# Optimization experiments

Hardware: AMD Instinct MI355X
Metric: run time of the kernel (lower is better)

Reference implementation:

```python
import jax, jax.numpy as jnp
import numpy as np

IN_DIM = 256
FF = 512
OUT_DIM = 256
BN_EPS = 1e-5


def setup_inputs() -> dict:
    key = jax.random.key(0)
    ks = jax.random.split(key, 9)
    s = lambda k, shape, fan: jax.random.normal(k, shape, dtype=jnp.float32) / np.sqrt(fan)
    return {
        "inputs": jax.random.normal(ks[0], (4, IN_DIM, 16, 16, 16), dtype=jnp.float32),
        "Wk": s(ks[1], (FF, IN_DIM), IN_DIM),
        "bk": jnp.zeros((FF,), jnp.float32),
        "Wq": s(ks[2], (FF, IN_DIM), IN_DIM),
        "bq": jnp.zeros((FF,), jnp.float32),
        "Wv": s(ks[3], (FF, IN_DIM), IN_DIM),
        "bv": jnp.zeros((FF,), jnp.float32),
        "Wo": s(ks[4], (OUT_DIM, FF), FF),
        "bo": jnp.zeros((OUT_DIM,), jnp.float32),
        "gamma": jnp.ones((OUT_DIM,), jnp.float32),
        "beta": jnp.zeros((OUT_DIM,), jnp.float32),
    }


def reference(inputs, Wk, bk, Wq, bq, Wv, bv, Wo, bo, gamma, beta):
    B, Cin, T, H, W = inputs.shape
    # 1x1x1 Conv3d == pointwise channel projection
    proj = lambda Wt, bt: jnp.einsum("oc,bcthw->bothw", Wt, inputs) + bt[None, :, None, None, None]
    K, Q, V = proj(Wk, bk), proj(Wq, bq), proj(Wv, bv)
    C = K.shape[1]
    N = T * H * W
    Kf = K.reshape(B, C, N)
    Qf = Q.reshape(B, C, N)
    Vf = V.reshape(B, C, N)
    # KQ[b,i,j] = sum_c K[b,c,i] Q[b,c,j], scaled by sqrt(in_dim) (per original)
    KQ = jnp.einsum("bci,bcj->bij", Kf, Qf) / jnp.sqrt(jnp.asarray(Cin, jnp.float32))
    attn = jax.nn.softmax(KQ, axis=2)  # (B, N, N)
    # Original: sum_j V[b,c,i] * attn[b,i,j]  ==  V[b,c,i] * rowsum(attn)[b,i]
    # (we avoid materializing the (B,C,N,N) broadcast tensor)
    row = attn.sum(axis=2)  # (B, N), ~1 numerically but kept for faithfulness
    Vagg = (Vf * row[:, None, :]).reshape(B, C, T, H, W)
    V1 = jax.nn.relu(Vagg)
    out = jnp.einsum("oc,bcthw->bothw", Wo, V1) + bo[None, :, None, None, None]
    res = inputs + jax.nn.relu(out)
    # BatchNorm3d in training mode: batch stats over (B, T, H, W) per channel
    mean = res.mean(axis=(0, 2, 3, 4), keepdims=True)
    var = res.var(axis=(0, 2, 3, 4), keepdims=True)
    xhat = (res - mean) * jax.lax.rsqrt(var + BN_EPS)
    return gamma[None, :, None, None, None] * xhat + beta[None, :, None, None, None]
```

## Files before the change

kernel.cpp:

```cpp
#include <hip/hip_runtime.h>

#define NTOT 4096
#define NB   4
#define CIN  256
#define FF   512
#define COUT 256
#define BN_EPS 1e-5f
#define NT_B 32
#define OSP  36

typedef __attribute__((ext_vector_type(8))) short bf16x8;
typedef __attribute__((ext_vector_type(4))) float f32x4;
typedef unsigned short u16;

#define MFMA16(A, B, C) __builtin_amdgcn_mfma_f32_16x16x32_bf16((A), (B), (C), 0, 0, 0)

__device__ __forceinline__ u16 f2bf(float f) {
    unsigned u = __float_as_uint(f);
    u += 0x7fffu + ((u >> 16) & 1u);
    return (u16)(u >> 16);
}
__device__ __forceinline__ float bf2f(u16 h) {
    return __uint_as_float(((unsigned)h) << 16);
}

__global__ __launch_bounds__(256)
void prep_weights(const float* __restrict__ Wv, const float* __restrict__ Wo,
                  u16* __restrict__ Wvh, u16* __restrict__ Wvl,
                  u16* __restrict__ Woh, u16* __restrict__ Wol,
                  float* __restrict__ stats)
{
    const int t = threadIdx.x;
    const int g = blockIdx.x * 256 + t;
    if (blockIdx.x == 0) { stats[t] = 0.f; stats[256 + t] = 0.f; }

    const float* src; u16 *dh, *dl; int m, kg, K;
    if (g < 16384) { m = g >> 5;           kg = g & 31; K = CIN; src = Wv; dh = Wvh; dl = Wvl; }
    else           { int g2 = g - 16384; m = g2 >> 6; kg = g2 & 63; K = FF;  src = Wo; dh = Woh; dl = Wol; }

    const int nkg = K >> 3;
    const size_t gran = ((size_t)(m >> 4) * nkg + kg) * 16 + (m & 15);
    float4 v0 = *(const float4*)&src[(size_t)m * K + kg * 8];
    float4 v1 = *(const float4*)&src[(size_t)m * K + kg * 8 + 4];
    const float f[8] = {v0.x, v0.y, v0.z, v0.w, v1.x, v1.y, v1.z, v1.w};
    u16 h[8], l[8];
    #pragma unroll
    for (int j = 0; j < 8; ++j) { h[j] = f2bf(f[j]); l[j] = f2bf(f[j] - bf2f(h[j])); }
    bf16x8 hv = {(short)h[0],(short)h[1],(short)h[2],(short)h[3],(short)h[4],(short)h[5],(short)h[6],(short)h[7]};
    bf16x8 lv = {(short)l[0],(short)l[1],(short)l[2],(short)l[3],(short)l[4],(short)l[5],(short)l[6],(short)l[7]};
    *(bf16x8*)&dh[gran * 8] = hv;
    *(bf16x8*)&dl[gran * 8] = lv;
}

__global__ __launch_bounds__(256)
void pack_x(const float* __restrict__ x, u16* __restrict__ xh, u16* __restrict__ xl)
{
    __shared__ float xt[CIN][68];
    const int t = threadIdx.x;
    const int b = blockIdx.x >> 6, tb = blockIdx.x & 63;
    const int n0 = tb * 64;
    const int c16 = t >> 4, tok4 = (t & 15) * 4;

    #pragma unroll
    for (int rr = 0; rr < 16; ++rr) {
        const int c = rr * 16 + c16;
        float4 v = *(const float4*)&x[((size_t)b * CIN + c) * NTOT + n0 + tok4];
        *(float4*)&xt[c][tok4] = v;
    }
    __syncthreads();

    const int tok = t & 63, wq = t >> 6;
    const int sb = tok >> 5, tok32 = tok & 31;
    #pragma unroll
    for (int r = 0; r < 8; ++r) {
        const int kg = r * 4 + wq;
        u16 h8[8], l8[8];
        #pragma unroll
        for (int j = 0; j < 8; ++j) {
            float f = xt[kg * 8 + j][tok];
            h8[j] = f2bf(f);
            l8[j] = f2bf(f - bf2f(h8[j]));
        }
        const size_t e = ((((size_t)(b * 128 + tb * 2 + sb)) * 32 + kg) * 32 + tok32) * 8;
        bf16x8 hv = {(short)h8[0],(short)h8[1],(short)h8[2],(short)h8[3],(short)h8[4],(short)h8[5],(short)h8[6],(short)h8[7]};
        bf16x8 lv = {(short)l8[0],(short)l8[1],(short)l8[2],(short)l8[3],(short)l8[4],(short)l8[5],(short)l8[6],(short)l8[7]};
        *(bf16x8*)&xh[e] = hv;
        *(bf16x8*)&xl[e] = lv;
    }
}

__global__ __launch_bounds__(512, 4)
void fused_mlp(const u16* __restrict__ xh, const u16* __restrict__ xl,
               const u16* __restrict__ Wvh, const u16* __restrict__ Wvl,
               const u16* __restrict__ Woh, const u16* __restrict__ Wol,
               const float* __restrict__ bv, const float* __restrict__ bo,
               const float* __restrict__ x, float* __restrict__ out,
               float* __restrict__ stats)
{
    __shared__ __align__(16) unsigned char smem[65536];
    u16*   xsh = (u16*)smem;
    u16*   xsl = (u16*)(smem + 16384);
    u16*   hsh = (u16*)smem;
    u16*   hsl = (u16*)(smem + 32768);
    float* os  = (float*)smem;

    const int t   = threadIdx.x;
    const int b   = blockIdx.x >> 7;
    const int tb2 = blockIdx.x & 127;
    const int n0  = tb2 * NT_B;
    const int ln  = t & 63, w = t >> 6;
    const int l15 = ln & 15, hi = ln >> 4;

    const size_t xbase = ((size_t)(b * 128 + tb2)) * 8192;
    #pragma unroll
    for (int i = 0; i < 2; ++i) {
        const int e = (i * 512 + t) * 8;
        *(bf16x8*)&xsh[e] = *(const bf16x8*)&xh[xbase + e];
        *(bf16x8*)&xsl[e] = *(const bf16x8*)&xl[xbase + e];
    }

    f32x4 acc1[4][2];
    #pragma unroll
    for (int mt = 0; mt < 4; ++mt)
        #pragma unroll
        for (int nt = 0; nt < 2; ++nt)
            acc1[mt][nt] = (f32x4){0.f, 0.f, 0.f, 0.f};

#define LDW1(KS, P, WH, WL) do { _Pragma("unroll")                              \
    for (int i_ = 0; i_ < 2; ++i_) {                                            \
        const int mt_ = (P) * 2 + i_;                                           \
        const size_t g_ = ((size_t)(w * 4 + mt_) * 32 + (KS) * 4 + hi) * 16 + l15; \
        WH[i_] = *(const bf16x8*)&Wvh[g_ * 8];                                  \
        WL[i_] = *(const bf16x8*)&Wvl[g_ * 8];                                  \
    } } while (0)
#define LDB1(KS, BH, BL) do { _Pragma("unroll")                                 \
    for (int nt_ = 0; nt_ < 2; ++nt_) {                                         \
        const int g_ = ((KS) * 4 + hi) * 32 + nt_ * 16 + l15;                   \
        BH[nt_] = *(const bf16x8*)&xsh[g_ * 8];                                 \
        BL[nt_] = *(const bf16x8*)&xsl[g_ * 8];                                 \
    } } while (0)
#define MM1(P, WH, WL, BH, BL) do { _Pragma("unroll")                           \
    for (int i_ = 0; i_ < 2; ++i_) { _Pragma("unroll")                          \
        for (int nt_ = 0; nt_ < 2; ++nt_) {                                     \
            acc1[(P)*2+i_][nt_] = MFMA16(WH[i_], BH[nt_], acc1[(P)*2+i_][nt_]); \
            acc1[(P)*2+i_][nt_] = MFMA16(WH[i_], BL[nt_], acc1[(P)*2+i_][nt_]); \
            acc1[(P)*2+i_][nt_] = MFMA16(WL[i_], BH[nt_], acc1[(P)*2+i_][nt_]); \
    } } } while (0)

    bf16x8 w1hA[2], w1lA[2], w1hB[2], w1lB[2];
    bf16x8 b1hE[2], b1lE[2], b1hO[2], b1lO[2];

    LDW1(0, 0, w1hA, w1lA);
    __syncthreads();
    LDB1(0, b1hE, b1lE);

    #pragma unroll
    for (int s = 0; s < 16; ++s) {
        const int ks = s >> 1, p = s & 1;
        if (p == 0) {
            LDW1(ks, 1, w1hB, w1lB);
        } else if (ks < 7) {
            LDW1(ks + 1, 0, w1hA, w1lA);
            if (ks & 1) { LDB1(ks + 1, b1hE, b1lE); }
            else        { LDB1(ks + 1, b1hO, b1lO); }
        }
        if (p == 0) {
            if (ks & 1) MM1(0, w1hA, w1lA, b1hO, b1lO);
            else        MM1(0, w1hA, w1lA, b1hE, b1lE);
        } else {
            if (ks & 1) MM1(1, w1hB, w1lB, b1hO, b1lO);
            else        MM1(1, w1hB, w1lB, b1hE, b1lE);
        }
    }
#undef LDW1
#undef LDB1
#undef MM1

#define LDW2(KS, WH, WL) do { _Pragma("unroll")                                 \
    for (int mt_ = 0; mt_ < 2; ++mt_) {                                         \
        const size_t g_ = ((size_t)(w * 2 + mt_) * 64 + (KS) * 4 + hi) * 16 + l15; \
        WH[mt_] = *(const bf16x8*)&Woh[g_ * 8];                                 \
        WL[mt_] = *(const bf16x8*)&Wol[g_ * 8];                                 \
    } } while (0)
#define LDB2(KS, BH, BL) do { _Pragma("unroll")                                 \
    for (int nt_ = 0; nt_ < 2; ++nt_) {                                         \
        const int g_ = ((KS) * 4 + hi) * 32 + nt_ * 16 + l15;                   \
        BH[nt_] = *(const bf16x8*)&hsh[g_ * 8];                                 \
        BL[nt_] = *(const bf16x8*)&hsl[g_ * 8];                                 \
    } } while (0)
#define MM2(WH, WL, BH, BL) do { _Pragma("unroll")                              \
    for (int mt_ = 0; mt_ < 2; ++mt_) { _Pragma("unroll")                       \
        for (int nt_ = 0; nt_ < 2; ++nt_) {                                     \
            acc2[mt_][nt_] = MFMA16(WH[mt_], BH[nt_], acc2[mt_][nt_]);          \
            acc2[mt_][nt_] = MFMA16(WH[mt_], BL[nt_], acc2[mt_][nt_]);          \
            acc2[mt_][nt_] = MFMA16(WL[mt_], BH[nt_], acc2[mt_][nt_]);          \
    } } } while (0)

    bf16x8 w2hA[2], w2lA[2], w2hB[2], w2lB[2];
    bf16x8 b2hE[2], b2lE[2], b2hO[2], b2lO[2];
    LDW2(0, w2hA, w2lA);

    __syncthreads();

    #pragma unroll
    for (int mt = 0; mt < 4; ++mt) {
        const int ff0 = w * 64 + mt * 16 + hi * 4;
        float4 bia = *(const float4*)&bv[ff0];
        const float bb[4] = {bia.x, bia.y, bia.z, bia.w};
        const int kg = ff0 >> 3;
        const int jo = (hi & 1) * 4;
        #pragma unroll
        for (int nt = 0; nt < 2; ++nt) {
            const int tok = nt * 16 + l15;
            u16 hh[4], hl[4];
            #pragma unroll
            for (int r = 0; r < 4; ++r) {
                float v = fmaxf(acc1[mt][nt][r] + bb[r], 0.f);
                hh[r] = f2bf(v);
                hl[r] = f2bf(v - bf2f(hh[r]));
            }
            const int e = (kg * 32 + tok) * 8 + jo;
            *(ushort4*)&hsh[e] = (ushort4){hh[0], hh[1], hh[2], hh[3]};
            *(ushort4*)&hsl[e] = (ushort4){hl[0], hl[1], hl[2], hl[3]};
        }
    }
    __syncthreads();

    f32x4 acc2[2][2];
    #pragma unroll
    for (int mt = 0; mt < 2; ++mt)
        #pragma unroll
        for (int nt = 0; nt < 2; ++nt)
            acc2[mt][nt] = (f32x4){0.f, 0.f, 0.f, 0.f};

    LDB2(0, b2hE, b2lE);
    #pragma unroll
    for (int ks = 0; ks < 16; ++ks) {
        if (ks < 15) {
            if (ks & 1) { LDW2(ks + 1, w2hA, w2lA); LDB2(ks + 1, b2hE, b2lE); }
            else        { LDW2(ks + 1, w2hB, w2lB); LDB2(ks + 1, b2hO, b2lO); }
        }
        if (ks & 1) MM2(w2hB, w2lB, b2hO, b2lO);
        else        MM2(w2hA, w2lA, b2hE, b2lE);
    }
#undef LDW2
#undef LDB2
#undef MM2

    __syncthreads();

    #pragma unroll
    for (int mt = 0; mt < 2; ++mt) {
        const int ch0 = w * 32 + mt * 16 + hi * 4;
        float4 bia = *(const float4*)&bo[ch0];
        const float bb[4] = {bia.x, bia.y, bia.z, bia.w};
        #pragma unroll
        for (int nt = 0; nt < 2; ++nt) {
            const int tok = nt * 16 + l15;
            #pragma unroll
            for (int r = 0; r < 4; ++r)
                os[(ch0 + r) * OSP + tok] = fmaxf(acc2[mt][nt][r] + bb[r], 0.f);
        }
    }
    __syncthreads();

    const int tok4 = (t & 7) * 4;
    const int chb  = t >> 3;
    #pragma unroll
    for (int ii = 0; ii < 4; ++ii) {
        const int ch = chb + ii * 64;
        float4 o = *(float4*)&os[ch * OSP + tok4];
        const size_t goff = ((size_t)b * COUT + ch) * NTOT + n0 + tok4;
        float4 rx = *(const float4*)&x[goff];
        float4 v = {o.x + rx.x, o.y + rx.y, o.z + rx.z, o.w + rx.w};
        *(float4*)&out[goff] = v;
        float s  = v.x + v.y + v.z + v.w;
        float s2 = v.x * v.x + v.y * v.y + v.z * v.z + v.w * v.w;
        #pragma unroll
        for (int off = 1; off < 8; off <<= 1) {
            s  += __shfl_xor(s, off);
            s2 += __shfl_xor(s2, off);
        }
        if ((t & 7) == 0) {
            atomicAdd(&stats[ch], s);
            atomicAdd(&stats[COUT + ch], s2);
        }
    }
}

__global__ __launch_bounds__(256)
void bn_norm(float* __restrict__ out, const float* __restrict__ stats,
             const float* __restrict__ gamma, const float* __restrict__ beta)
{
    const int i4 = blockIdx.x * 256 + threadIdx.x;
    const int c = (i4 >> 10) & (COUT - 1);
    const float inv = 1.0f / (NB * NTOT);
    const float mean = stats[c] * inv;
    const float var  = stats[COUT + c] * inv - mean * mean;
    const float sc = gamma[c] * rsqrtf(var + BN_EPS);
    const float sh = beta[c] - mean * sc;
    float4 v = reinterpret_cast<float4*>(out)[i4];
    v.x = v.x * sc + sh;
    v.y = v.y * sc + sh;
    v.z = v.z * sc + sh;
    v.w = v.w * sc + sh;
    reinterpret_cast<float4*>(out)[i4] = v;
}

extern "C" void kernel_launch(void* const* d_in, const int* in_sizes, int n_in,
                              void* d_out, int out_size, void* d_ws, size_t ws_size,
                              hipStream_t stream)
{
    const float* x     = (const float*)d_in[0];
    const float* Wv    = (const float*)d_in[5];
    const float* bv    = (const float*)d_in[6];
    const float* Wo    = (const float*)d_in[7];
    const float* bo    = (const float*)d_in[8];
    const float* gamma = (const float*)d_in[9];
    const float* beta  = (const float*)d_in[10];
    float* out = (float*)d_out;

    u16* xh   = (u16*)d_ws;
    u16* xl   = xh  + (size_t)NB * NTOT * CIN;
    u16* Wvh  = xl  + (size_t)NB * NTOT * CIN;
    u16* Wvl  = Wvh + (size_t)FF * CIN;
    u16* Woh  = Wvl + (size_t)FF * CIN;
    u16* Wol  = Woh + (size_t)COUT * FF;
    float* stats = (float*)(Wol + (size_t)COUT * FF);

    prep_weights<<<128, 256, 0, stream>>>(Wv, Wo, Wvh, Wvl, Woh, Wol, stats);
    pack_x<<<NB * 64, 256, 0, stream>>>(x, xh, xl);
    fused_mlp<<<NB * 128, 512, 0, stream>>>(xh, xl, Wvh, Wvl, Woh, Wol,
                                            bv, bo, x, out, stats);
    bn_norm<<<(NB * COUT * NTOT / 4) / 256, 256, 0, stream>>>(out, stats, gamma, beta);
}
```

Before: 159.0 us.

## Fuse x bf16 hi/lo packing into fused_mlp and drop pack_x kernel

Removes the separate pack_x kernel and instead has each fused_mlp block load its fp32 input tile straight from global memory into shared memory, then split it into bf16 hi/lo parts in LDS before the MFMA loop. This cuts one kernel launch and the global write and re-read of the packed hi/lo buffers. In exchange it adds an extra __syncthreads and conversion work inside the main kernel, and puts the raw tile and the packed tiles in LDS at the same time.

```diff
diff --git a/kernel.cpp b/kernel.cpp
--- a/kernel.cpp
+++ b/kernel.cpp
@@ -52,54 +52,17 @@
     *(bf16x8*)&dl[gran * 8] = lv;
 }
 
-__global__ __launch_bounds__(256)
-void pack_x(const float* __restrict__ x, u16* __restrict__ xh, u16* __restrict__ xl)
-{
-    __shared__ float xt[CIN][68];
-    const int t = threadIdx.x;
-    const int b = blockIdx.x >> 6, tb = blockIdx.x & 63;
-    const int n0 = tb * 64;
-    const int c16 = t >> 4, tok4 = (t & 15) * 4;
-
-    #pragma unroll
-    for (int rr = 0; rr < 16; ++rr) {
-        const int c = rr * 16 + c16;
-        float4 v = *(const float4*)&x[((size_t)b * CIN + c) * NTOT + n0 + tok4];
-        *(float4*)&xt[c][tok4] = v;
-    }
-    __syncthreads();
-
-    const int tok = t & 63, wq = t >> 6;
-    const int sb = tok >> 5, tok32 = tok & 31;
-    #pragma unroll
-    for (int r = 0; r < 8; ++r) {
-        const int kg = r * 4 + wq;
-        u16 h8[8], l8[8];
-        #pragma unroll
-        for (int j = 0; j < 8; ++j) {
-            float f = xt[kg * 8 + j][tok];
-            h8[j] = f2bf(f);
-            l8[j] = f2bf(f - bf2f(h8[j]));
-        }
-        const size_t e = ((((size_t)(b * 128 + tb * 2 + sb)) * 32 + kg) * 32 + tok32) * 8;
-        bf16x8 hv = {(short)h8[0],(short)h8[1],(short)h8[2],(short)h8[3],(short)h8[4],(short)h8[5],(short)h8[6],(short)h8[7]};
-        bf16x8 lv = {(short)l8[0],(short)l8[1],(short)l8[2],(short)l8[3],(short)l8[4],(short)l8[5],(short)l8[6],(short)l8[7]};
-        *(bf16x8*)&xh[e] = hv;
-        *(bf16x8*)&xl[e] = lv;
-    }
-}
-
 __global__ __launch_bounds__(512, 4)
-void fused_mlp(const u16* __restrict__ xh, const u16* __restrict__ xl,
+void fused_mlp(const float* __restrict__ x,
                const u16* __restrict__ Wvh, const u16* __restrict__ Wvl,
                const u16* __restrict__ Woh, const u16* __restrict__ Wol,
                const float* __restrict__ bv, const float* __restrict__ bo,
-               const float* __restrict__ x, float* __restrict__ out,
-               float* __restrict__ stats)
+               float* __restrict__ out, float* __restrict__ stats)
 {
     __shared__ __align__(16) unsigned char smem[65536];
-    u16*   xsh = (u16*)smem;
-    u16*   xsl = (u16*)(smem + 16384);
+    float* xt  = (float*)smem;
+    u16*   xsh = (u16*)(smem + 32768);
+    u16*   xsl = (u16*)(smem + 49152);
     u16*   hsh = (u16*)smem;
     u16*   hsl = (u16*)(smem + 32768);
     float* os  = (float*)smem;
@@ -111,20 +74,13 @@
     const int ln  = t & 63, w = t >> 6;
     const int l15 = ln & 15, hi = ln >> 4;
 
-    const size_t xbase = ((size_t)(b * 128 + tb2)) * 8192;
-    #pragma unroll
-    for (int i = 0; i < 2; ++i) {
-        const int e = (i * 512 + t) * 8;
-        *(bf16x8*)&xsh[e] = *(const bf16x8*)&xh[xbase + e];
-        *(bf16x8*)&xsl[e] = *(const bf16x8*)&xl[xbase + e];
-    }
-
-    f32x4 acc1[4][2];
-    #pragma unroll
-    for (int mt = 0; mt < 4; ++mt)
-        #pragma unroll
-        for (int nt = 0; nt < 2; ++nt)
-            acc1[mt][nt] = (f32x4){0.f, 0.f, 0.f, 0.f};
+    #pragma unroll
+    for (int i = 0; i < 4; ++i) {
+        const int f4 = t + i * 512;
+        const int c = f4 >> 3, col4 = (f4 & 7) * 4;
+        float4 v = *(const float4*)&x[((size_t)b * CIN + c) * NTOT + n0 + col4];
+        *(float4*)&xt[c * NT_B + col4] = v;
+    }
 
 #define LDW1(KS, P, WH, WL) do { _Pragma("unroll")                              \
     for (int i_ = 0; i_ < 2; ++i_) {                                            \
@@ -133,6 +89,39 @@
         WH[i_] = *(const bf16x8*)&Wvh[g_ * 8];                                  \
         WL[i_] = *(const bf16x8*)&Wvl[g_ * 8];                                  \
     } } while (0)
+
+    bf16x8 w1hA[2], w1lA[2], w1hB[2], w1lB[2];
+    LDW1(0, 0, w1hA, w1lA);
+    __syncthreads();
+
+    {
+        const int tok = t & 31, kg0 = t >> 5;
+        #pragma unroll
+        for (int i = 0; i < 2; ++i) {
+            const int kg = kg0 + i * 16;
+            u16 h8[8], l8[8];
+            #pragma unroll
+            for (int j = 0; j < 8; ++j) {
+                float f = xt[(kg * 8 + j) * NT_B + tok];
+                h8[j] = f2bf(f);
+                l8[j] = f2bf(f - bf2f(h8[j]));
+            }
+            const int e = (kg * 32 + tok) * 8;
+            bf16x8 hv = {(short)h8[0],(short)h8[1],(short)h8[2],(short)h8[3],(short)h8[4],(short)h8[5],(short)h8[6],(short)h8[7]};
+            bf16x8 lv = {(short)l8[0],(short)l8[1],(short)l8[2],(short)l8[3],(short)l8[4],(short)l8[5],(short)l8[6],(short)l8[7]};
+            *(bf16x8*)&xsh[e] = hv;
+            *(bf16x8*)&xsl[e] = lv;
+        }
+    }
+    __syncthreads();
+
+    f32x4 acc1[4][2];
+    #pragma unroll
+    for (int mt = 0; mt < 4; ++mt)
+        #pragma unroll
+        for (int nt = 0; nt < 2; ++nt)
+            acc1[mt][nt] = (f32x4){0.f, 0.f, 0.f, 0.f};
+
 #define LDB1(KS, BH, BL) do { _Pragma("unroll")                                 \
     for (int nt_ = 0; nt_ < 2; ++nt_) {                                         \
         const int g_ = ((KS) * 4 + hi) * 32 + nt_ * 16 + l15;                   \
@@ -147,11 +136,7 @@
             acc1[(P)*2+i_][nt_] = MFMA16(WL[i_], BH[nt_], acc1[(P)*2+i_][nt_]); \
     } } } while (0)
 
-    bf16x8 w1hA[2], w1lA[2], w1hB[2], w1lB[2];
     bf16x8 b1hE[2], b1lE[2], b1hO[2], b1lO[2];
-
-    LDW1(0, 0, w1hA, w1lA);
-    __syncthreads();
     LDB1(0, b1hE, b1lE);
 
     #pragma unroll
@@ -320,17 +305,14 @@
     const float* beta  = (const float*)d_in[10];
     float* out = (float*)d_out;
 
-    u16* xh   = (u16*)d_ws;
-    u16* xl   = xh  + (size_t)NB * NTOT * CIN;
-    u16* Wvh  = xl  + (size_t)NB * NTOT * CIN;
+    u16* Wvh  = (u16*)d_ws;
     u16* Wvl  = Wvh + (size_t)FF * CIN;
     u16* Woh  = Wvl + (size_t)FF * CIN;
     u16* Wol  = Woh + (size_t)COUT * FF;
     float* stats = (float*)(Wol + (size_t)COUT * FF);
 
     prep_weights<<<128, 256, 0, stream>>>(Wv, Wo, Wvh, Wvl, Woh, Wol, stats);
-    pack_x<<<NB * 64, 256, 0, stream>>>(x, xh, xl);
-    fused_mlp<<<NB * 128, 512, 0, stream>>>(xh, xl, Wvh, Wvl, Woh, Wol,
-                                            bv, bo, x, out, stats);
+    fused_mlp<<<NB * 128, 512, 0, stream>>>(x, Wvh, Wvl, Woh, Wol,
+                                            bv, bo, out, stats);
     bn_norm<<<(NB * COUT * NTOT / 4) / 256, 256, 0, stream>>>(out, stats, gamma, beta);
 }
```

Measured after the change: 152.2 us. 1.04x faster.
